# Optimization experiments

Hardware: AMD Instinct MI355X
Metric: run time of the kernel (lower is better)

Reference implementation:

```python
import jax, jax.numpy as jnp
import numpy as np
import math

NUM_HEADS = 16
SIZE = 1024
HEAD_SIZE = SIZE // NUM_HEADS
B, S = 2, 2048


def setup_inputs() -> dict:
    key = jax.random.key(0)
    ks = jax.random.split(key, 11)
    sc = 1.0 / math.sqrt(SIZE)
    inp = {
        "q": jax.random.normal(ks[0], (B, S, SIZE), dtype=jnp.float32),
        "k": jax.random.normal(ks[1], (B, S, SIZE), dtype=jnp.float32),
        "v": jax.random.normal(ks[2], (B, S, SIZE), dtype=jnp.float32),
        "Wq": jax.random.normal(ks[3], (SIZE, SIZE), dtype=jnp.float32) * sc,
        "bq": jax.random.normal(ks[4], (SIZE,), dtype=jnp.float32) * sc,
        "Wk": jax.random.normal(ks[5], (SIZE, SIZE), dtype=jnp.float32) * sc,
        "bk": jax.random.normal(ks[6], (SIZE,), dtype=jnp.float32) * sc,
        "Wv": jax.random.normal(ks[7], (SIZE, SIZE), dtype=jnp.float32) * sc,
        "bv": jax.random.normal(ks[8], (SIZE,), dtype=jnp.float32) * sc,
        "Wo": jax.random.normal(ks[9], (SIZE, SIZE), dtype=jnp.float32) * sc,
        "bo": jax.random.normal(ks[10], (SIZE,), dtype=jnp.float32) * sc,
    }
    return inp


def _split_heads(x):
    # [B, S, SIZE] -> [B, H, S, D]
    b, s, _ = x.shape
    return x.reshape(b, s, NUM_HEADS, HEAD_SIZE).transpose(0, 2, 1, 3)


def reference(q, k, v, Wq, bq, Wk, bk, Wv, bv, Wo, bo):
    qh = _split_heads(q @ Wq.T + bq) / math.sqrt(HEAD_SIZE)  # [B,H,S,D]
    kh = _split_heads(k @ Wk.T + bk)
    vh = _split_heads(v @ Wv.T + bv)
    scores = jnp.einsum("bhqd,bhkd->bhqk", qh, kh)  # [B,H,S,S]
    attn = jax.nn.softmax(scores, axis=-1)
    ctx = jnp.einsum("bhqk,bhkd->bhqd", attn, vh)  # [B,H,S,D]
    ctx = ctx.transpose(0, 2, 1, 3).reshape(q.shape[0], -1, SIZE)
    return ctx @ Wo.T + bo
```

## Files before the change

kernel.cpp:

```cpp
#include <hip/hip_runtime.h>
#include <hip/hip_bf16.h>

#define SIZE 1024
#define NH 16
#define HD 64
#define BB 2
#define SS 2048
#define MROWS (BB * SS)
#define QT 256
#define NQT (SS / QT)
#define NKT ((SS / 2) / 64)

using bf16 = __hip_bfloat16;
using frag16 = __attribute__((ext_vector_type(8))) short;
using f32x4 = __attribute__((ext_vector_type(4))) float;
typedef unsigned int u32;

__device__ __forceinline__ void glds16(const bf16* g, bf16* l) {
    __builtin_amdgcn_global_load_lds(
        (const __attribute__((address_space(1))) u32*)g,
        (__attribute__((address_space(3))) u32*)l, 16, 0, 0);
}

__device__ __forceinline__ void cvt_store8(bf16* dst, const float* src) {
    float4 a = *(const float4*)src;
    float4 b = *(const float4*)(src + 4);
    bf16 t[8];
    t[0] = __float2bfloat16(a.x); t[1] = __float2bfloat16(a.y);
    t[2] = __float2bfloat16(a.z); t[3] = __float2bfloat16(a.w);
    t[4] = __float2bfloat16(b.x); t[5] = __float2bfloat16(b.y);
    t[6] = __float2bfloat16(b.z); t[7] = __float2bfloat16(b.w);
    *(uint4*)dst = *(const uint4*)t;
}

__global__ __launch_bounds__(256) void cast_kernel(
    const float* __restrict__ Wq, const float* __restrict__ Wk,
    const float* __restrict__ Wv, const float* __restrict__ Wo,
    const float* __restrict__ q, const float* __restrict__ k,
    const float* __restrict__ v,
    bf16* __restrict__ Wb, bf16* __restrict__ qb,
    bf16* __restrict__ kb, bf16* __restrict__ vb)
{
    const size_t WN = (size_t)SIZE * SIZE;
    const size_t AN = (size_t)MROWS * SIZE;
    const size_t e = ((size_t)blockIdx.x * 256 + threadIdx.x) * 8;
    if (e < 4 * WN) {
        const int which = (int)(e >> 20);
        const size_t off = e & (WN - 1);
        const float* s = (which == 0) ? Wq : (which == 1) ? Wk : (which == 2) ? Wv : Wo;
        cvt_store8(Wb + e, s + off);
    } else {
        const size_t a = e - 4 * WN;
        const int which = (int)(a >> 22);
        const size_t off = a & (AN - 1);
        const float* s = (which == 0) ? q : (which == 1) ? k : v;
        bf16* d = (which == 0) ? qb : (which == 1) ? kb : vb;
        cvt_store8(d + off, s + off);
    }
}

__device__ __forceinline__ void gemm_body(
    const bf16* __restrict__ X, const bf16* __restrict__ W,
    const float* __restrict__ bias, bf16* __restrict__ Y, float scale, bool vt_mode,
    int bm, int bn)
{
    __shared__ __align__(16) bf16 smem[16384];
    bf16* As = smem;
    bf16* Bs = smem + 8192;

    const int tid = threadIdx.x;
    const int wave = tid >> 6;
    const int lane = tid & 63;
    const int lane15 = lane & 15;
    const int quad = lane >> 4;
    const int wm = (wave & 1) * 64;
    const int wn = (wave >> 1) * 64;

    f32x4 acc[4][4];
#pragma unroll
    for (int i = 0; i < 4; i++)
#pragma unroll
        for (int j = 0; j < 4; j++)
            acc[i][j] = (f32x4){0.f, 0.f, 0.f, 0.f};

    const int srow = lane >> 2;
    const int scol = (lane & 3) * 8;

#define STAGE(KT, BUF)                                                         \
    {                                                                          \
        _Pragma("unroll")                                                      \
        for (int n = 0; n < 2; n++) {                                          \
            const int c = wave * 2 + n;          \
            glds16(X + (size_t)(bm + c * 16 + srow) * SIZE + (KT) * 32 + scol, \
                   As + (BUF) * 4096 + c * 512);                               \
            glds16(W + (size_t)(bn + c * 16 + srow) * SIZE + (KT) * 32 + scol, \
                   Bs + (BUF) * 4096 + c * 512);                               \
        }                                                                      \
    }

    STAGE(0, 0);
    __syncthreads();

    for (int kt = 0; kt < SIZE / 32; kt++) {
        const int buf = kt & 1;
        if (kt + 1 < SIZE / 32) STAGE(kt + 1, buf ^ 1);
        __builtin_amdgcn_sched_barrier(0);

        frag16 a[4], b[4];
#pragma unroll
        for (int mi = 0; mi < 4; mi++)
            a[mi] = *(const frag16*)(As + buf * 4096 + (wm + mi * 16 + lane15) * 32 + quad * 8);
#pragma unroll
        for (int ni = 0; ni < 4; ni++)
            b[ni] = *(const frag16*)(Bs + buf * 4096 + (wn + ni * 16 + lane15) * 32 + quad * 8);
#pragma unroll
        for (int mi = 0; mi < 4; mi++)
#pragma unroll
            for (int ni = 0; ni < 4; ni++)
                acc[mi][ni] = __builtin_amdgcn_mfma_f32_16x16x32_bf16(
                    a[mi], b[ni], acc[mi][ni], 0, 0, 0);

        __syncthreads();
    }
#undef STAGE

    if (!vt_mode) {
#pragma unroll
        for (int ni = 0; ni < 4; ni++) {
            const int col = bn + wn + ni * 16 + lane15;
            const float bv = bias[col];
#pragma unroll
            for (int mi = 0; mi < 4; mi++) {
                const int row = bm + wm + mi * 16 + quad * 4;
#pragma unroll
                for (int r = 0; r < 4; r++)
                    Y[(size_t)(row + r) * SIZE + col] =
                        __float2bfloat16((acc[mi][ni][r] + bv) * scale);
            }
        }
    } else {
        bf16* tr = smem;
        const int bloc = bm >> 11;
        const int s0g = bm & (SS - 1);
#pragma unroll
        for (int p = 0; p < 2; p++) {
            __syncthreads();
            if ((wave >> 1) == p) {
#pragma unroll
                for (int ni = 0; ni < 4; ni++) {
                    const int colp = ni * 16 + lane15;
                    const float bv = bias[bn + p * 64 + colp];
#pragma unroll
                    for (int mi = 0; mi < 4; mi++) {
                        const int row = wm + mi * 16 + quad * 4;
#pragma unroll
                        for (int r = 0; r < 4; r++)
                            tr[colp * 136 + row + r] =
                                __float2bfloat16(acc[mi][ni][r] + bv);
                    }
                }
            }
            __syncthreads();
            const int colp = tid >> 2;
            const int gcol = bn + p * 64 + colp;
            const int hh = gcol >> 6, dd = gcol & (HD - 1);
            bf16* dst = (bf16*)Y + ((size_t)(bloc * NH + hh) * HD + dd) * SS
                        + s0g + (tid & 3) * 32;
            const bf16* src = tr + colp * 136 + (tid & 3) * 32;
#pragma unroll
            for (int j = 0; j < 4; j++)
                *(uint4*)(dst + j * 8) = *(const uint4*)(src + j * 8);
        }
    }
}

__global__ __launch_bounds__(256) void qkv_proj_kernel(
    const bf16* __restrict__ qb, const bf16* __restrict__ kb, const bf16* __restrict__ vb,
    const bf16* __restrict__ Wb,
    const float* __restrict__ bq, const float* __restrict__ bk, const float* __restrict__ bv,
    bf16* __restrict__ qh, bf16* __restrict__ kh, bf16* __restrict__ vt)
{
    const int f = blockIdx.x;
    const int w = (f & 7) * 96 + (f >> 3);
    const int z = w >> 8;
    const int rem = w & 255;
    const int bn = (rem & 7) * 128;
    const int bm = (rem >> 3) * 128;

    const bf16 *X, *W; const float* bi; bf16* Y; float sc; bool vm;
    if (z == 0)      { X = qb; W = Wb;                   bi = bq; Y = qh; sc = 0.125f; vm = false; }
    else if (z == 1) { X = kb; W = Wb + SIZE * SIZE;     bi = bk; Y = kh; sc = 1.0f;   vm = false; }
    else             { X = vb; W = Wb + 2 * SIZE * SIZE; bi = bv; Y = vt; sc = 1.0f;   vm = true;  }
    gemm_body(X, W, bi, Y, sc, vm, bm, bn);
}

__global__ __launch_bounds__(256) void attn_kernel(
    const bf16* __restrict__ qh, const bf16* __restrict__ kh,
    const bf16* __restrict__ vt, bf16* __restrict__ po, float* __restrict__ pl)
{
    __shared__ __align__(16) bf16 Ks[2][64][72];
    __shared__ __align__(16) bf16 Vs[2][64][72];
    __shared__ __align__(16) bf16 Ps[4][64][72];

    const int tid = threadIdx.x;
    const int wave = tid >> 6;
    const int lane = tid & 63;
    const int lane15 = lane & 15;
    const int quad = lane >> 4;

    const int b = blockIdx.z, h = blockIdx.y;
    const int qt = blockIdx.x >> 1;
    const int sh = blockIdx.x & 1;
    const int q0 = qt * QT;

    const size_t baseq = (size_t)b * SS * SIZE + (size_t)h * HD;
    const size_t basev = (size_t)(b * NH + h) * HD * SS;
    const float LOG2E = 1.44269504088896340736f;
    const float OFF = 12.0f * LOG2E;

    frag16 aq[4][2];
#pragma unroll
    for (int m = 0; m < 4; m++) {
        const int qrow = q0 + wave * 64 + m * 16 + lane15;
        const bf16* qp = qh + baseq + (size_t)qrow * SIZE + quad * 8;
        aq[m][0] = *(const frag16*)(qp);
        aq[m][1] = *(const frag16*)(qp + 32);
    }

    frag16 bones;
#pragma unroll
    for (int e = 0; e < 8; e++) bones[e] = (short)0x3F80;

    f32x4 ofrag[4][4], l_frag[4];
#pragma unroll
    for (int m = 0; m < 4; m++) {
        l_frag[m] = (f32x4){0.f, 0.f, 0.f, 0.f};
#pragma unroll
        for (int dt = 0; dt < 4; dt++) ofrag[m][dt] = (f32x4){0.f, 0.f, 0.f, 0.f};
    }

    const int sr = tid >> 3;
    const int sc = (tid & 7) * 8;

    uint4 rk0, rk1, rv0, rv1;

#define ISSUE(KT)                                                              \
    {                                                                          \
        const int s0_ = sh * (SS / 2) + (KT) * 64;                             \
        rk0 = *(const uint4*)(kh + baseq + (size_t)(s0_ + sr) * SIZE + sc);    \
        rk1 = *(const uint4*)(kh + baseq + (size_t)(s0_ + sr + 32) * SIZE + sc);\
        rv0 = *(const uint4*)(vt + basev + (size_t)sr * SS + s0_ + sc);        \
        rv1 = *(const uint4*)(vt + basev + (size_t)(sr + 32) * SS + s0_ + sc); \
    }
#define COMMIT(BUF)                                                            \
    {                                                                          \
        *(uint4*)&Ks[BUF][sr][sc] = rk0; *(uint4*)&Ks[BUF][sr + 32][sc] = rk1; \
        *(uint4*)&Vs[BUF][sr][sc] = rv0; *(uint4*)&Vs[BUF][sr + 32][sc] = rv1; \
    }

    ISSUE(0); COMMIT(0);
    __syncthreads();

    for (int kt = 0; kt < NKT; kt++) {
        const int buf = kt & 1;
        if (kt + 1 < NKT) ISSUE(kt + 1);
        __builtin_amdgcn_sched_barrier(0);

        frag16 kf[4][2];
#pragma unroll
        for (int nt = 0; nt < 4; nt++) {
            kf[nt][0] = *(const frag16*)&Ks[buf][nt * 16 + lane15][quad * 8];
            kf[nt][1] = *(const frag16*)&Ks[buf][nt * 16 + lane15][32 + quad * 8];
        }
#pragma unroll
        for (int m = 0; m < 4; m++) {
#pragma unroll
            for (int nt = 0; nt < 4; nt++) {
                f32x4 c = (f32x4){0.f, 0.f, 0.f, 0.f};
                c = __builtin_amdgcn_mfma_f32_16x16x32_bf16(kf[nt][0], aq[m][0], c, 0, 0, 0);
                c = __builtin_amdgcn_mfma_f32_16x16x32_bf16(kf[nt][1], aq[m][1], c, 0, 0, 0);
                bf16 p4[4];
#pragma unroll
                for (int r = 0; r < 4; r++)
                    p4[r] = __float2bfloat16(exp2f(c[r] * LOG2E - OFF));
                *(uint2*)&Ps[wave][m * 16 + lane15][nt * 16 + quad * 4] = *(const uint2*)p4;
            }
        }
        __builtin_amdgcn_wave_barrier();

        frag16 ap[4][2];
#pragma unroll
        for (int m = 0; m < 4; m++)
#pragma unroll
            for (int c2 = 0; c2 < 2; c2++)
                ap[m][c2] = *(const frag16*)&Ps[wave][m * 16 + lane15][c2 * 32 + quad * 8];

        __builtin_amdgcn_s_setprio(1);
#pragma unroll
        for (int m = 0; m < 4; m++)
#pragma unroll
            for (int c2 = 0; c2 < 2; c2++)
                l_frag[m] = __builtin_amdgcn_mfma_f32_16x16x32_bf16(
                    ap[m][c2], bones, l_frag[m], 0, 0, 0);

#pragma unroll
        for (int dt = 0; dt < 4; dt++) {
            frag16 bv0 = *(const frag16*)&Vs[buf][dt * 16 + lane15][quad * 8];
            frag16 bv1 = *(const frag16*)&Vs[buf][dt * 16 + lane15][32 + quad * 8];
#pragma unroll
            for (int m = 0; m < 4; m++) {
                ofrag[m][dt] = __builtin_amdgcn_mfma_f32_16x16x32_bf16(ap[m][0], bv0, ofrag[m][dt], 0, 0, 0);
                ofrag[m][dt] = __builtin_amdgcn_mfma_f32_16x16x32_bf16(ap[m][1], bv1, ofrag[m][dt], 0, 0, 0);
            }
        }
        __builtin_amdgcn_s_setprio(0);

        if (kt + 1 < NKT) {
            COMMIT(buf ^ 1);
            __syncthreads();
        }
    }
#undef ISSUE
#undef COMMIT

    const int pb = ((b * NH + h) * NQT + qt) * 2 + sh;
    if (lane15 == 0) {
        float* plp = pl + (size_t)pb * QT;
#pragma unroll
        for (int m = 0; m < 4; m++)
#pragma unroll
            for (int r = 0; r < 4; r++)
                plp[wave * 64 + m * 16 + quad * 4 + r] = l_frag[m][r];
    }
    bf16* pop = po + (size_t)pb * QT * HD;
#pragma unroll
    for (int m = 0; m < 4; m++)
#pragma unroll
        for (int dt = 0; dt < 4; dt++)
#pragma unroll
            for (int r = 0; r < 4; r++)
                pop[(size_t)(wave * 64 + m * 16 + quad * 4 + r) * HD + dt * 16 + lane15] =
                    __float2bfloat16(ofrag[m][dt][r]);
}

__global__ __launch_bounds__(256) void out_proj_kernel(
    const bf16* __restrict__ po, const float* __restrict__ pl,
    const bf16* __restrict__ Wob, const float* __restrict__ bo,
    float* __restrict__ out)
{
    __shared__ __align__(16) bf16 As[2 * 64 * 32];
    __shared__ __align__(16) bf16 Bs[2 * 128 * 32];

    const int f = blockIdx.x;
    const int w = (f & 7) * 64 + (f >> 3);
    const int bn = (w & 7) * 128;
    const int bm = (w >> 3) * 64;

    const int tid = threadIdx.x;
    const int wave = tid >> 6;
    const int lane = tid & 63;
    const int lane15 = lane & 15;
    const int quad = lane >> 4;
    const int wn = wave * 32;

    f32x4 acc[4][2];
#pragma unroll
    for (int i = 0; i < 4; i++)
#pragma unroll
        for (int j = 0; j < 2; j++)
            acc[i][j] = (f32x4){0.f, 0.f, 0.f, 0.f};

    const int srow = lane >> 2;
    const int scol = (lane & 3) * 8;

    const int arow = tid >> 2;
    const int acol = (tid & 3) * 8;
    const int gr = bm + arow;
    const int bIdx = gr >> 11;
    const int s = gr & (SS - 1);
    const int qt8 = s >> 8;
    const int sq = s & (QT - 1);

    uint4 p0a, p1a, p0b, p1b;
    float l0, l1;

#define ALOAD(KT)                                                                 \
    {                                                                             \
        const int pb0_ = ((bIdx * NH + (KT)) * NQT + qt8) * 2;                    \
        const bf16* q0_ = po + (size_t)pb0_ * QT * HD + sq * HD;                  \
        const bf16* q1_ = po + (size_t)(pb0_ + 1) * QT * HD + sq * HD;            \
        p0a = *(const uint4*)(q0_ + acol);                                        \
        p0b = *(const uint4*)(q0_ + 32 + acol);                                   \
        p1a = *(const uint4*)(q1_ + acol);                                        \
        p1b = *(const uint4*)(q1_ + 32 + acol);                                   \
        l0 = pl[(size_t)pb0_ * QT + sq];                                          \
        l1 = pl[(size_t)(pb0_ + 1) * QT + sq];                                    \
    }

    ALOAD(0);

    for (int kt = 0; kt < NH; kt++) {
        __syncthreads();
        {
            const float inv = 1.0f / fmaxf(l0 + l1, 1e-30f);
            const bf16* x0 = (const bf16*)&p0a; const bf16* y0 = (const bf16*)&p1a;
            const bf16* x1 = (const bf16*)&p0b; const bf16* y1 = (const bf16*)&p1b;
            bf16 o0[8], o1[8];
#pragma unroll
            for (int e = 0; e < 8; e++) {
                o0[e] = __float2bfloat16((__bfloat162float(x0[e]) + __bfloat162float(y0[e])) * inv);
                o1[e] = __float2bfloat16((__bfloat162float(x1[e]) + __bfloat162float(y1[e])) * inv);
            }
            *(uint4*)(As + 0 * 2048 + arow * 32 + acol) = *(const uint4*)o0;
            *(uint4*)(As + 1 * 2048 + arow * 32 + acol) = *(const uint4*)o1;
        }
#pragma unroll
        for (int n = 0; n < 4; n++) {
            const int c = wave * 4 + n;
            const int plane = c >> 3;
            const int cc = c & 7;
            glds16(Wob + (size_t)(bn + cc * 16 + srow) * SIZE + kt * 64 + plane * 32 + scol,
                   Bs + c * 512);
        }
        __syncthreads();

        if (kt + 1 < NH) ALOAD(kt + 1);

#pragma unroll
        for (int kk = 0; kk < 2; kk++) {
            frag16 a[4], b[2];
#pragma unroll
            for (int mi = 0; mi < 4; mi++)
                a[mi] = *(const frag16*)(As + kk * 2048 + (mi * 16 + lane15) * 32 + quad * 8);
#pragma unroll
            for (int ni = 0; ni < 2; ni++)
                b[ni] = *(const frag16*)(Bs + kk * 4096 + (wn + ni * 16 + lane15) * 32 + quad * 8);
#pragma unroll
            for (int mi = 0; mi < 4; mi++)
#pragma unroll
                for (int ni = 0; ni < 2; ni++)
                    acc[mi][ni] = __builtin_amdgcn_mfma_f32_16x16x32_bf16(
                        a[mi], b[ni], acc[mi][ni], 0, 0, 0);
        }
    }
#undef ALOAD

#pragma unroll
    for (int ni = 0; ni < 2; ni++) {
        const int col = bn + wn + ni * 16 + lane15;
        const float bv = bo[col];
#pragma unroll
        for (int mi = 0; mi < 4; mi++) {
            const int row = bm + mi * 16 + quad * 4;
#pragma unroll
            for (int r = 0; r < 4; r++)
                out[(size_t)(row + r) * SIZE + col] = acc[mi][ni][r] + bv;
        }
    }
}

extern "C" void kernel_launch(void* const* d_in, const int* in_sizes, int n_in,
                              void* d_out, int out_size, void* d_ws, size_t ws_size,
                              hipStream_t stream) {
    const float* q  = (const float*)d_in[0];
    const float* k  = (const float*)d_in[1];
    const float* v  = (const float*)d_in[2];
    const float* Wq = (const float*)d_in[3];
    const float* bq = (const float*)d_in[4];
    const float* Wk = (const float*)d_in[5];
    const float* bk = (const float*)d_in[6];
    const float* Wv = (const float*)d_in[7];
    const float* bv = (const float*)d_in[8];
    const float* Wo = (const float*)d_in[9];
    const float* bo = (const float*)d_in[10];
    float* out = (float*)d_out;

    bf16* Wb  = (bf16*)d_ws;
    bf16* qb  = Wb + (size_t)4 * SIZE * SIZE;
    bf16* kb  = qb + (size_t)MROWS * SIZE;
    bf16* vb  = kb + (size_t)MROWS * SIZE;
    bf16* qh  = vb + (size_t)MROWS * SIZE;
    bf16* kh  = qh + (size_t)MROWS * SIZE;
    bf16* vt  = kh + (size_t)MROWS * SIZE;
    bf16* po  = qb;
    float* pl = (float*)Wb;

    cast_kernel<<<dim3(8192, 1, 1), 256, 0, stream>>>(
        Wq, Wk, Wv, Wo, q, k, v, Wb, qb, kb, vb);
    qkv_proj_kernel<<<dim3(768, 1, 1), 256, 0, stream>>>(
        qb, kb, vb, Wb, bq, bk, bv, qh, kh, vt);
    attn_kernel<<<dim3(NQT * 2, NH, BB), 256, 0, stream>>>(qh, kh, vt, po, pl);
    out_proj_kernel<<<dim3(512, 1, 1), 256, 0, stream>>>(
        po, pl, Wb + (size_t)3 * SIZE * SIZE, bo, out);
}
```

Measured before the change: 248.9 us.

## Load K/V fragments directly from global memory and remap attention grid for XCD locality

Removes the shared-memory double-buffered K/V staging in the attention kernel, so each wave loads its MFMA K and V fragments straight from global memory and the block-wide barriers go away. The grid becomes 1D with a swizzled block index, so blocks sharing the same (batch, head) K/V land on the same XCD's L2. The trade-off is that every one of the four waves now fetches the same K/V data separately, which relies on cache hits. It also loses explicit prefetch overlap, so global-load latency sits directly ahead of the MFMAs.

```diff
diff --git a/kernel.cpp b/kernel.cpp
--- a/kernel.cpp
+++ b/kernel.cpp
@@ -198,8 +198,6 @@
     const bf16* __restrict__ qh, const bf16* __restrict__ kh,
     const bf16* __restrict__ vt, bf16* __restrict__ po, float* __restrict__ pl)
 {
-    __shared__ __align__(16) bf16 Ks[2][64][72];
-    __shared__ __align__(16) bf16 Vs[2][64][72];
     __shared__ __align__(16) bf16 Ps[4][64][72];
 
     const int tid = threadIdx.x;
@@ -208,9 +206,14 @@
     const int lane15 = lane & 15;
     const int quad = lane >> 4;
 
-    const int b = blockIdx.z, h = blockIdx.y;
-    const int qt = blockIdx.x >> 1;
-    const int sh = blockIdx.x & 1;
+    const int f = blockIdx.x;
+    const int w = (f & 7) * 64 + (f >> 3);
+    const int bh = w >> 4;
+    const int within = w & 15;
+    const int b = bh >> 4;
+    const int h = bh & 15;
+    const int qt = within >> 1;
+    const int sh = within & 1;
     const int q0 = qt * QT;
 
     const size_t baseq = (size_t)b * SS * SIZE + (size_t)h * HD;
@@ -239,39 +242,26 @@
         for (int dt = 0; dt < 4; dt++) ofrag[m][dt] = (f32x4){0.f, 0.f, 0.f, 0.f};
     }
 
-    const int sr = tid >> 3;
-    const int sc = (tid & 7) * 8;
-
-    uint4 rk0, rk1, rv0, rv1;
-
-#define ISSUE(KT)                                                              \
-    {                                                                          \
-        const int s0_ = sh * (SS / 2) + (KT) * 64;                             \
-        rk0 = *(const uint4*)(kh + baseq + (size_t)(s0_ + sr) * SIZE + sc);    \
-        rk1 = *(const uint4*)(kh + baseq + (size_t)(s0_ + sr + 32) * SIZE + sc);\
-        rv0 = *(const uint4*)(vt + basev + (size_t)sr * SS + s0_ + sc);        \
-        rv1 = *(const uint4*)(vt + basev + (size_t)(sr + 32) * SS + s0_ + sc); \
-    }
-#define COMMIT(BUF)                                                            \
-    {                                                                          \
-        *(uint4*)&Ks[BUF][sr][sc] = rk0; *(uint4*)&Ks[BUF][sr + 32][sc] = rk1; \
-        *(uint4*)&Vs[BUF][sr][sc] = rv0; *(uint4*)&Vs[BUF][sr + 32][sc] = rv1; \
-    }
-
-    ISSUE(0); COMMIT(0);
-    __syncthreads();
+    const bf16* kbase = kh + baseq + (size_t)(sh * (SS / 2) + lane15) * SIZE + quad * 8;
+    const bf16* vbase = vt + basev + (size_t)lane15 * SS + sh * (SS / 2) + quad * 8;
 
     for (int kt = 0; kt < NKT; kt++) {
-        const int buf = kt & 1;
-        if (kt + 1 < NKT) ISSUE(kt + 1);
-        __builtin_amdgcn_sched_barrier(0);
-
-        frag16 kf[4][2];
+        const int s0 = kt * 64;
+
+        frag16 kf[4][2], bv[4][2];
 #pragma unroll
         for (int nt = 0; nt < 4; nt++) {
-            kf[nt][0] = *(const frag16*)&Ks[buf][nt * 16 + lane15][quad * 8];
-            kf[nt][1] = *(const frag16*)&Ks[buf][nt * 16 + lane15][32 + quad * 8];
-        }
+            const bf16* kp = kbase + (size_t)(s0 + nt * 16) * SIZE;
+            kf[nt][0] = *(const frag16*)(kp);
+            kf[nt][1] = *(const frag16*)(kp + 32);
+        }
+#pragma unroll
+        for (int dt = 0; dt < 4; dt++) {
+            const bf16* vp = vbase + (size_t)(dt * 16) * SS + s0;
+            bv[dt][0] = *(const frag16*)(vp);
+            bv[dt][1] = *(const frag16*)(vp + 32);
+        }
+
 #pragma unroll
         for (int m = 0; m < 4; m++) {
 #pragma unroll
@@ -305,23 +295,14 @@
 
 #pragma unroll
         for (int dt = 0; dt < 4; dt++) {
-            frag16 bv0 = *(const frag16*)&Vs[buf][dt * 16 + lane15][quad * 8];
-            frag16 bv1 = *(const frag16*)&Vs[buf][dt * 16 + lane15][32 + quad * 8];
 #pragma unroll
             for (int m = 0; m < 4; m++) {
-                ofrag[m][dt] = __builtin_amdgcn_mfma_f32_16x16x32_bf16(ap[m][0], bv0, ofrag[m][dt], 0, 0, 0);
-                ofrag[m][dt] = __builtin_amdgcn_mfma_f32_16x16x32_bf16(ap[m][1], bv1, ofrag[m][dt], 0, 0, 0);
+                ofrag[m][dt] = __builtin_amdgcn_mfma_f32_16x16x32_bf16(ap[m][0], bv[dt][0], ofrag[m][dt], 0, 0, 0);
+                ofrag[m][dt] = __builtin_amdgcn_mfma_f32_16x16x32_bf16(ap[m][1], bv[dt][1], ofrag[m][dt], 0, 0, 0);
             }
         }
         __builtin_amdgcn_s_setprio(0);
-
-        if (kt + 1 < NKT) {
-            COMMIT(buf ^ 1);
-            __syncthreads();
-        }
-    }
-#undef ISSUE
-#undef COMMIT
+    }
 
     const int pb = ((b * NH + h) * NQT + qt) * 2 + sh;
     if (lane15 == 0) {
@@ -489,7 +470,7 @@
         Wq, Wk, Wv, Wo, q, k, v, Wb, qb, kb, vb);
     qkv_proj_kernel<<<dim3(768, 1, 1), 256, 0, stream>>>(
         qb, kb, vb, Wb, bq, bk, bv, qh, kh, vt);
-    attn_kernel<<<dim3(NQT * 2, NH, BB), 256, 0, stream>>>(qh, kh, vt, po, pl);
+    attn_kernel<<<dim3(512, 1, 1), 256, 0, stream>>>(qh, kh, vt, po, pl);
     out_proj_kernel<<<dim3(512, 1, 1), 256, 0, stream>>>(
         po, pl, Wb + (size_t)3 * SIZE * SIZE, bo, out);
 }
```

After: 255.9 us. 1.03x slower.

## Use 32x32 MFMA in attention with register-resident P via permlane swap

Applied to the files above, without the earlier changes.

Rewrites the attention inner loop to use 32x32x16 bf16 MFMAs. The exp'd scores are converted with packed bf16 conversion and rearranged into A-operand layout with permlane32_swap, so the LDS round-trip for P is gone. The row sum is now accumulated in scalar registers instead of a ones-vector MFMA, and blocks are remapped through a swizzled 1D grid. This cuts LDS traffic and MFMA issue count, in exchange for higher register pressure and layout-sensitive fragment shuffles.

```diff
diff --git a/kernel.cpp b/kernel.cpp
--- a/kernel.cpp
+++ b/kernel.cpp
@@ -14,7 +14,9 @@
 using bf16 = __hip_bfloat16;
 using frag16 = __attribute__((ext_vector_type(8))) short;
 using f32x4 = __attribute__((ext_vector_type(4))) float;
+using f32x16 = __attribute__((ext_vector_type(16))) float;
 typedef unsigned int u32;
+typedef __attribute__((ext_vector_type(4))) unsigned int u32x4v;
 
 __device__ __forceinline__ void glds16(const bf16* g, bf16* l) {
     __builtin_amdgcn_global_load_lds(
@@ -200,17 +202,21 @@
 {
     __shared__ __align__(16) bf16 Ks[2][64][72];
     __shared__ __align__(16) bf16 Vs[2][64][72];
-    __shared__ __align__(16) bf16 Ps[4][64][72];
 
     const int tid = threadIdx.x;
     const int wave = tid >> 6;
     const int lane = tid & 63;
-    const int lane15 = lane & 15;
-    const int quad = lane >> 4;
-
-    const int b = blockIdx.z, h = blockIdx.y;
-    const int qt = blockIdx.x >> 1;
-    const int sh = blockIdx.x & 1;
+    const int L31 = lane & 31;
+    const int t8 = (lane >> 5) * 8;
+
+    const int f = blockIdx.x;
+    const int w = (f & 7) * 64 + (f >> 3);
+    const int bh = w >> 4;
+    const int within = w & 15;
+    const int b = bh >> 4;
+    const int h = bh & 15;
+    const int qt = within >> 1;
+    const int sh = within & 1;
     const int q0 = qt * QT;
 
     const size_t baseq = (size_t)b * SS * SIZE + (size_t)h * HD;
@@ -218,32 +224,30 @@
     const float LOG2E = 1.44269504088896340736f;
     const float OFF = 12.0f * LOG2E;
 
-    frag16 aq[4][2];
-#pragma unroll
-    for (int m = 0; m < 4; m++) {
-        const int qrow = q0 + wave * 64 + m * 16 + lane15;
-        const bf16* qp = qh + baseq + (size_t)qrow * SIZE + quad * 8;
-        aq[m][0] = *(const frag16*)(qp);
-        aq[m][1] = *(const frag16*)(qp + 32);
-    }
-
-    frag16 bones;
-#pragma unroll
-    for (int e = 0; e < 8; e++) bones[e] = (short)0x3F80;
-
-    f32x4 ofrag[4][4], l_frag[4];
-#pragma unroll
-    for (int m = 0; m < 4; m++) {
-        l_frag[m] = (f32x4){0.f, 0.f, 0.f, 0.f};
-#pragma unroll
-        for (int dt = 0; dt < 4; dt++) ofrag[m][dt] = (f32x4){0.f, 0.f, 0.f, 0.f};
-    }
+    frag16 aq[2][4];
+#pragma unroll
+    for (int m2 = 0; m2 < 2; m2++) {
+        const bf16* qp = qh + baseq
+            + (size_t)(q0 + wave * 64 + m2 * 32 + L31) * SIZE + t8;
+#pragma unroll
+        for (int kk = 0; kk < 4; kk++)
+            aq[m2][kk] = *(const frag16*)(qp + kk * 16);
+    }
+
+    f32x16 ofrag[2][2];
+#pragma unroll
+    for (int m2 = 0; m2 < 2; m2++)
+#pragma unroll
+        for (int d2 = 0; d2 < 2; d2++)
+#pragma unroll
+            for (int r = 0; r < 16; r++)
+                ofrag[m2][d2][r] = 0.f;
+    float lsc[2] = {0.f, 0.f};
 
     const int sr = tid >> 3;
     const int sc = (tid & 7) * 8;
 
     uint4 rk0, rk1, rv0, rv1;
-
 #define ISSUE(KT)                                                              \
     {                                                                          \
         const int s0_ = sh * (SS / 2) + (KT) * 64;                             \
@@ -266,54 +270,67 @@
         if (kt + 1 < NKT) ISSUE(kt + 1);
         __builtin_amdgcn_sched_barrier(0);
 
-        frag16 kf[4][2];
-#pragma unroll
-        for (int nt = 0; nt < 4; nt++) {
-            kf[nt][0] = *(const frag16*)&Ks[buf][nt * 16 + lane15][quad * 8];
-            kf[nt][1] = *(const frag16*)&Ks[buf][nt * 16 + lane15][32 + quad * 8];
-        }
-#pragma unroll
-        for (int m = 0; m < 4; m++) {
-#pragma unroll
-            for (int nt = 0; nt < 4; nt++) {
-                f32x4 c = (f32x4){0.f, 0.f, 0.f, 0.f};
-                c = __builtin_amdgcn_mfma_f32_16x16x32_bf16(kf[nt][0], aq[m][0], c, 0, 0, 0);
-                c = __builtin_amdgcn_mfma_f32_16x16x32_bf16(kf[nt][1], aq[m][1], c, 0, 0, 0);
-                bf16 p4[4];
-#pragma unroll
-                for (int r = 0; r < 4; r++)
-                    p4[r] = __float2bfloat16(exp2f(c[r] * LOG2E - OFF));
-                *(uint2*)&Ps[wave][m * 16 + lane15][nt * 16 + quad * 4] = *(const uint2*)p4;
+#pragma unroll
+        for (int n2 = 0; n2 < 2; n2++) {
+            frag16 kfr[4];
+#pragma unroll
+            for (int kk = 0; kk < 4; kk++)
+                kfr[kk] = *(const frag16*)&Ks[buf][n2 * 32 + L31][kk * 16 + t8];
+
+            frag16 pa[2][2];
+#pragma unroll
+            for (int m2 = 0; m2 < 2; m2++) {
+                f32x16 c;
+#pragma unroll
+                for (int r = 0; r < 16; r++) c[r] = 0.f;
+#pragma unroll
+                for (int kk = 0; kk < 4; kk++)
+                    c = __builtin_amdgcn_mfma_f32_32x32x16_bf16(
+                        kfr[kk], aq[m2][kk], c, 0, 0, 0);
+                float p[16];
+                float s = 0.f;
+#pragma unroll
+                for (int r = 0; r < 16; r++) {
+                    p[r] = exp2f(c[r] * LOG2E - OFF);
+                    s += p[r];
+                }
+                lsc[m2] += s;
+                u32 wv[4][2];
+#pragma unroll
+                for (int s4 = 0; s4 < 4; s4++)
+#pragma unroll
+                    for (int j = 0; j < 2; j++)
+                        asm("v_cvt_pk_bf16_f32 %0, %1, %2"
+                            : "=v"(wv[s4][j])
+                            : "v"(p[s4 * 4 + 2 * j]), "v"(p[s4 * 4 + 2 * j + 1]));
+#pragma unroll
+                for (int kk2 = 0; kk2 < 2; kk2++) {
+                    u32x4v wd;
+#pragma unroll
+                    for (int j = 0; j < 2; j++) {
+                        auto rr = __builtin_amdgcn_permlane32_swap(
+                            wv[2 * kk2][j], wv[2 * kk2 + 1][j], false, false);
+                        wd[j] = rr[0];
+                        wd[2 + j] = rr[1];
+                    }
+                    pa[m2][kk2] = __builtin_bit_cast(frag16, wd);
+                }
             }
-        }
-        __builtin_amdgcn_wave_barrier();
-
-        frag16 ap[4][2];
-#pragma unroll
-        for (int m = 0; m < 4; m++)
-#pragma unroll
-            for (int c2 = 0; c2 < 2; c2++)
-                ap[m][c2] = *(const frag16*)&Ps[wave][m * 16 + lane15][c2 * 32 + quad * 8];
-
-        __builtin_amdgcn_s_setprio(1);
-#pragma unroll
-        for (int m = 0; m < 4; m++)
-#pragma unroll
-            for (int c2 = 0; c2 < 2; c2++)
-                l_frag[m] = __builtin_amdgcn_mfma_f32_16x16x32_bf16(
-                    ap[m][c2], bones, l_frag[m], 0, 0, 0);
-
-#pragma unroll
-        for (int dt = 0; dt < 4; dt++) {
-            frag16 bv0 = *(const frag16*)&Vs[buf][dt * 16 + lane15][quad * 8];
-            frag16 bv1 = *(const frag16*)&Vs[buf][dt * 16 + lane15][32 + quad * 8];
-#pragma unroll
-            for (int m = 0; m < 4; m++) {
-                ofrag[m][dt] = __builtin_amdgcn_mfma_f32_16x16x32_bf16(ap[m][0], bv0, ofrag[m][dt], 0, 0, 0);
-                ofrag[m][dt] = __builtin_amdgcn_mfma_f32_16x16x32_bf16(ap[m][1], bv1, ofrag[m][dt], 0, 0, 0);
-            }
-        }
-        __builtin_amdgcn_s_setprio(0);
+
+            __builtin_amdgcn_s_setprio(1);
+#pragma unroll
+            for (int kk2 = 0; kk2 < 2; kk2++)
+#pragma unroll
+                for (int d2 = 0; d2 < 2; d2++) {
+                    frag16 vfr = *(const frag16*)
+                        &Vs[buf][d2 * 32 + L31][n2 * 32 + kk2 * 16 + t8];
+#pragma unroll
+                    for (int m2 = 0; m2 < 2; m2++)
+                        ofrag[m2][d2] = __builtin_amdgcn_mfma_f32_32x32x16_bf16(
+                            pa[m2][kk2], vfr, ofrag[m2][d2], 0, 0, 0);
+                }
+            __builtin_amdgcn_s_setprio(0);
+        }
 
         if (kt + 1 < NKT) {
             COMMIT(buf ^ 1);
@@ -324,23 +341,27 @@
 #undef COMMIT
 
     const int pb = ((b * NH + h) * NQT + qt) * 2 + sh;
-    if (lane15 == 0) {
+    {
         float* plp = pl + (size_t)pb * QT;
 #pragma unroll
-        for (int m = 0; m < 4; m++)
-#pragma unroll
-            for (int r = 0; r < 4; r++)
-                plp[wave * 64 + m * 16 + quad * 4 + r] = l_frag[m][r];
+        for (int m2 = 0; m2 < 2; m2++) {
+            const float ltot = lsc[m2] + __shfl_xor(lsc[m2], 32);
+            if (lane < 32)
+                plp[wave * 64 + m2 * 32 + L31] = ltot;
+        }
     }
     bf16* pop = po + (size_t)pb * QT * HD;
-#pragma unroll
-    for (int m = 0; m < 4; m++)
-#pragma unroll
-        for (int dt = 0; dt < 4; dt++)
-#pragma unroll
-            for (int r = 0; r < 4; r++)
-                pop[(size_t)(wave * 64 + m * 16 + quad * 4 + r) * HD + dt * 16 + lane15] =
-                    __float2bfloat16(ofrag[m][dt][r]);
+    const int t4 = (lane >> 5) * 4;
+#pragma unroll
+    for (int m2 = 0; m2 < 2; m2++)
+#pragma unroll
+        for (int d2 = 0; d2 < 2; d2++)
+#pragma unroll
+            for (int r = 0; r < 16; r++) {
+                const int row = wave * 64 + m2 * 32 + (r & 3) + 8 * (r >> 2) + t4;
+                pop[(size_t)row * HD + d2 * 32 + L31] =
+                    __float2bfloat16(ofrag[m2][d2][r]);
+            }
 }
 
 __global__ __launch_bounds__(256) void out_proj_kernel(
@@ -489,7 +510,7 @@
         Wq, Wk, Wv, Wo, q, k, v, Wb, qb, kb, vb);
     qkv_proj_kernel<<<dim3(768, 1, 1), 256, 0, stream>>>(
         qb, kb, vb, Wb, bq, bk, bv, qh, kh, vt);
-    attn_kernel<<<dim3(NQT * 2, NH, BB), 256, 0, stream>>>(qh, kh, vt, po, pl);
+    attn_kernel<<<dim3(512, 1, 1), 256, 0, stream>>>(qh, kh, vt, po, pl);
     out_proj_kernel<<<dim3(512, 1, 1), 256, 0, stream>>>(
         po, pl, Wb + (size_t)3 * SIZE * SIZE, bo, out);
 }
```

New measurement: 248.0 us. About the same (-0.4%).
